# Optimization experiments

Measured on AMD Instinct MI355X. Metric: run time of the kernel, lower is better.

## Reference

```python
import jax, jax.numpy as jnp
import numpy as np

T, B = 10, 512
N_ALL, N_AGENTS = 23, 22
N_FEAT = 4
X_DIM = 4
Z_EACH = 4
Z_DIM = N_ALL * Z_EACH  # 92
RNN_H = 64
NH = 8
E = N_ALL * (N_ALL - 1)  # 506

# edge list equivalent of the dense one-hot rel_rec / rel_send matrices
_off = np.ones((N_ALL, N_ALL)) - np.eye(N_ALL)
_recv_np, _send_np = np.where(_off)
RECV = jnp.asarray(_recv_np)  # rel_rec one-hot rows -> receiver node ids
SEND = jnp.asarray(_send_np)  # rel_send one-hot rows -> sender node ids
_et = np.zeros((E, 2), np.float32)
_et[np.arange(0, E, N_ALL - 1)[1:-1], 0] = 1.0
_et[-(N_ALL - 1):, 1] = 1.0
EDGE_TYPE = jnp.asarray(_et)
_nt = np.zeros((N_ALL, 2), np.float32)
_nt[:-1, 0] = 1.0
_nt[-1, 1] = 1.0
NODE_TYPE = jnp.asarray(_nt)


def _bn(x, g, b):
    # BatchNorm1d in training mode over flattened (B*M, C), biased variance
    B_, M, C = x.shape
    xf = x.reshape(B_ * M, C)
    mu = xf.mean(0)
    var = jnp.var(xf, axis=0)
    return ((xf - mu) * jax.lax.rsqrt(var + 1e-5) * g + b).reshape(B_, M, C)


def _mlp(x, W1, b1, W2, b2, g, bt):
    h = jax.nn.elu(jnp.einsum('bmi,hi->bmh', x, W1) + b1)
    h = jax.nn.elu(jnp.einsum('bmi,hi->bmh', h, W2) + b2)
    return _bn(h, g, bt)


def _kld(me, se, mp_, sp):
    return 0.5 * jnp.sum(2.0 * jnp.log(sp / se) + (se ** 2 + (me - mp_) ** 2) / sp ** 2 - 1.0)


def _gru_cell(Wih, Whh, bih, bhh, x, h):
    gi = x @ Wih.T + bih
    gh = h @ Whh.T + bhh
    ir, iz, inn = jnp.split(gi, 3, -1)
    hr, hz, hn = jnp.split(gh, 3, -1)
    r = jax.nn.sigmoid(ir + hr)
    z = jax.nn.sigmoid(iz + hz)
    n = jnp.tanh(inn + r * hn)
    return (1.0 - z) * n + z * h


_gru = jax.vmap(_gru_cell)  # over agents


def _forward(states, eps, mlp1_W1, mlp1_b1, mlp1_W2, mlp1_b2, mlp1_g, mlp1_beta,
             mlp2_W1, mlp2_b1, mlp2_W2, mlp2_b2, mlp2_g, mlp2_beta,
             mlp3_W1, mlp3_b1, mlp3_W2, mlp3_b2, mlp3_g, mlp3_beta,
             enc_mean_W, enc_mean_b, enc_std_W, enc_std_b,
             prior_mean_W, prior_mean_b, prior_std_W, prior_std_b,
             dec_mean_W, dec_mean_b, dec_std_W, dec_std_b,
             gru_Wih, gru_Whh, gru_bih, gru_bhh):
    Bsz = states.shape[2]
    y = states[:T, 0].reshape(T, Bsz, N_ALL, N_FEAT)        # y_t
    x1 = states[1:T + 1, 0].reshape(T, Bsz, N_ALL, N_FEAT)  # x_{t+1}
    P1 = (mlp1_W1, mlp1_b1, mlp1_W2, mlp1_b2, mlp1_g, mlp1_beta)
    P2 = (mlp2_W1, mlp2_b1, mlp2_W2, mlp2_b2, mlp2_g, mlp2_beta)
    P3 = (mlp3_W1, mlp3_b1, mlp3_W2, mlp3_b2, mlp3_g, mlp3_beta)

    def gnn(x, p):
        x = _mlp(x, *(a[p] for a in P1))
        # node2edge: gather senders/receivers instead of one-hot matmul
        e = jnp.concatenate([x[:, SEND], x[:, RECV],
                             jnp.broadcast_to(EDGE_TYPE, (Bsz, E, 2))], -1)
        e = _mlp(e, *(a[p] for a in P2))
        # edge2node: scatter-add into receiver nodes (rel_rec.T @ e)
        inc = jnp.zeros((Bsz, N_ALL, NH), x.dtype).at[:, RECV].add(e)
        inc = jnp.concatenate([inc, jnp.broadcast_to(NODE_TYPE, (Bsz, N_ALL, 2))], -1) / N_ALL
        return _mlp(inc, *(a[p] for a in P3))

    def step(carry, xs):
        h, Lkl = carry
        y_t, x_t, eps_t = xs
        micro = jnp.transpose(h, (1, 0, 2)).reshape(Bsz, -1)  # (B, nA*H)
        pri = jnp.concatenate([gnn(y_t, 0).reshape(Bsz, -1), micro], 1)
        enc = jnp.concatenate([gnn(x_t, 1).reshape(Bsz, -1), micro], 1)
        pm = pri @ prior_mean_W.T + prior_mean_b
        ps = jax.nn.softplus(pri @ prior_std_W.T + prior_std_b)
        em = enc @ enc_mean_W.T + enc_mean_b
        es = jax.nn.softplus(enc @ enc_std_W.T + enc_std_b)
        z = em + es * eps_t  # reparameterized sample_gauss
        Lkl = Lkl + _kld(em, es, pm, ps)
        z_ = z.reshape(Bsz, N_ALL, Z_EACH)
        dg = gnn(z_, 2).reshape(Bsz, -1)
        dm = dg @ dec_mean_W.T + dec_mean_b
        ds = jax.nn.softplus(dg @ dec_std_W.T + dec_std_b)
        # per-agent GRU update: input = [x_t agent feats, z slice]
        gin = jnp.transpose(
            jnp.concatenate([x_t[:, :N_AGENTS, :X_DIM], z_[:, :N_AGENTS]], -1), (1, 0, 2))
        h = _gru(gru_Wih, gru_Whh, gru_bih, gru_bhh, gin, h)
        return (h, Lkl), (dm, ds)

    h0 = jnp.zeros((N_AGENTS, Bsz, RNN_H), states.dtype)
    (_, Lkl), (dms, dss) = jax.lax.scan(step, (h0, jnp.zeros((), states.dtype)), (y, x1, eps))
    return dms, dss, Lkl


def setup_inputs() -> dict:
    key = jax.random.key(0)
    ks = iter(jax.random.split(key, 64))

    def rn(shape, s=0.1):
        return jax.random.normal(next(ks), shape, jnp.float32) * s

    d = {}
    d['states'] = rn((T + 1, 1, B, N_ALL * N_FEAT), 1.0)
    d['eps'] = rn((T, B, Z_DIM), 1.0)
    for i, nin in ((1, N_FEAT), (2, 2 * NH + 2), (3, NH + 2)):
        d['mlp%d_W1' % i] = rn((3, NH, nin), 0.3)
        d['mlp%d_b1' % i] = jnp.full((3, NH), 0.1, jnp.float32)
        d['mlp%d_W2' % i] = rn((3, NH, NH), 0.3)
        d['mlp%d_b2' % i] = jnp.full((3, NH), 0.1, jnp.float32)
        d['mlp%d_g' % i] = jnp.ones((3, NH), jnp.float32)
        d['mlp%d_beta' % i] = jnp.zeros((3, NH), jnp.float32)
    IN_H = NH * N_ALL + RNN_H * N_AGENTS  # 1592
    for nm in ('enc_mean', 'enc_std', 'prior_mean', 'prior_std'):
        d[nm + '_W'] = rn((Z_DIM, IN_H), 0.02)
        d[nm + '_b'] = jnp.zeros((Z_DIM,), jnp.float32)
    OUT_DEC = NH * N_ALL  # 184
    for nm in ('dec_mean', 'dec_std'):
        d[nm + '_W'] = rn((X_DIM * N_AGENTS, OUT_DEC), 0.05)
        d[nm + '_b'] = jnp.zeros((X_DIM * N_AGENTS,), jnp.float32)
    d['gru_Wih'] = rn((N_AGENTS, 3 * RNN_H, X_DIM + Z_EACH), 0.2)
    d['gru_Whh'] = rn((N_AGENTS, 3 * RNN_H, RNN_H), 0.1)
    d['gru_bih'] = jnp.zeros((N_AGENTS, 3 * RNN_H), jnp.float32)
    d['gru_bhh'] = jnp.zeros((N_AGENTS, 3 * RNN_H), jnp.float32)
    return d


def reference(states, eps, mlp1_W1, mlp1_b1, mlp1_W2, mlp1_b2, mlp1_g, mlp1_beta,
              mlp2_W1, mlp2_b1, mlp2_W2, mlp2_b2, mlp2_g, mlp2_beta,
              mlp3_W1, mlp3_b1, mlp3_W2, mlp3_b2, mlp3_g, mlp3_beta,
              enc_mean_W, enc_mean_b, enc_std_W, enc_std_b,
              prior_mean_W, prior_mean_b, prior_std_W, prior_std_b,
              dec_mean_W, dec_mean_b, dec_std_W, dec_std_b,
              gru_Wih, gru_Whh, gru_bih, gru_bhh):
    return _forward(states, eps, mlp1_W1, mlp1_b1, mlp1_W2, mlp1_b2, mlp1_g, mlp1_beta,
                    mlp2_W1, mlp2_b1, mlp2_W2, mlp2_b2, mlp2_g, mlp2_beta,
                    mlp3_W1, mlp3_b1, mlp3_W2, mlp3_b2, mlp3_g, mlp3_beta,
                    enc_mean_W, enc_mean_b, enc_std_W, enc_std_b,
                    prior_mean_W, prior_mean_b, prior_std_W, prior_std_b,
                    dec_mean_W, dec_mean_b, dec_std_W, dec_std_b,
                    gru_Wih, gru_Whh, gru_bih, gru_bhh)
```

## Files before the change

kernel.cpp:

```cpp
#include <hip/hip_runtime.h>
#include <hip/hip_bf16.h>
#include <math.h>


typedef __attribute__((ext_vector_type(8))) short s16x8;
typedef __attribute__((ext_vector_type(4))) float f32x4;

__device__ __forceinline__ unsigned short f2bf(float x){
  __hip_bfloat16 b = __float2bfloat16(x);
  return *reinterpret_cast<unsigned short*>(&b);
}
__device__ __forceinline__ float elu_(float x){ return x>0.f ? x : __expf(x)-1.f; }
__device__ __forceinline__ float sp_(float x){ return fmaxf(x,0.f)+log1pf(__expf(-fabsf(x))); }
__device__ __forceinline__ float sig_(float x){ return 1.f/(1.f+__expf(-x)); }
__device__ __forceinline__ float wsum_(float v){
  #pragma unroll
  for (int o=32;o;o>>=1) v += __shfl_down(v,o,64);
  return v;
}

__device__ __forceinline__ void reduce_bn_(const float* __restrict__ part, int n,
    float invN, const float* __restrict__ gam, const float* __restrict__ bet,
    float* sc, float* sh, float* tmp)
{
// ... 17 lines not shown
    float s2 = rs*gam[tid];
    sc[tid] = s2; sh[tid] = bet[tid] - m*s2;
  }
  __syncthreads();
}

__device__ __forceinline__ void block_stats_(const float h[8], float* __restrict__ part,
                                             float red[][16])
{
  int wid = threadIdx.x >> 6, lane = threadIdx.x & 63;
  #pragma unroll
  for (int j=0;j<8;j++){
    float a = wsum_(h[j]);
    float b = wsum_(h[j]*h[j]);
    if (lane==0){ red[wid][j]=a; red[wid][8+j]=b; }
  }
  __syncthreads();
  if (threadIdx.x < 16)
    part[threadIdx.x] = red[0][threadIdx.x]+red[1][threadIdx.x]
                       +red[2][threadIdx.x]+red[3][threadIdx.x];
}


__device__ __forceinline__ void dev_heads_mfma(
    int idx, int t,
    const unsigned short* __restrict__ g3b,
    const unsigned short* __restrict__ hb,
    const unsigned short* __restrict__ Wbt,
    const unsigned short* __restrict__ Wbs,
    const float* __restrict__ cst,
    float* __restrict__ raw)
{
  int head = idx & 3, mb = idx >> 2;
  int tid = threadIdx.x;
  int wv = tid >> 6, lane = tid & 63;
  int m0 = mb*64 + wv*16;
  int rloc = lane & 15, kg = lane >> 4;
  int row = m0 + rloc;
  int selg = (head < 2) ? t : 10 + t;
  const unsigned short* Ag = g3b + (size_t)selg*98304 + (size_t)row*192 + kg*8;
  const unsigned short* Wt = Wbt + (size_t)((t*4+head)*96)*192 + kg*8;
  const unsigned short* Wsb = Wbs + (size_t)head*135168;
  f32x4 cd[6];
  #pragma unroll
  for (int n=0;n<6;n++) cd[n] = (f32x4){0.f,0.f,0.f,0.f};
  #pragma unroll
  for (int ks=0; ks<6; ks++){
    s16x8 af = *(const s16x8*)(Ag + ks*32);
    #pragma unroll
    for (int n=0;n<6;n++){
      int col = n*16 + rloc;
      s16x8 bf = *(const s16x8*)(Wt + (size_t)col*192 + ks*32);
      cd[n] = __builtin_amdgcn_mfma_f32_16x16x32_bf16(af, bf, cd[n], 0,0,0);
    }
  }
  const unsigned short* Ah = hb + (size_t)row*64;
  #pragma unroll 4
  for (int ks=0; ks<44; ks++){
    int f2 = ks*32 + kg*8;
    s16x8 af = *(const s16x8*)(Ah + (size_t)(f2>>6)*32768 + (f2&63));
    #pragma unroll
    for (int n=0;n<6;n++){
      int col = n*16 + rloc;
      s16x8 bf = *(const s16x8*)(Wsb + (size_t)col*1408 + f2);
      cd[n] = __builtin_amdgcn_mfma_f32_16x16x32_bf16(af, bf, cd[n], 0,0,0);
    }
  }
  float* dst = raw + (size_t)head*47104;
  const float* cb = cst + (size_t)(t*4+head)*96;
  #pragma unroll
  for (int n=0;n<6;n++){
    int col = n*16 + rloc;
    if (col < 92){
      float cc = cb[col];
      #pragma unroll
      for (int r=0;r<4;r++){
        int rr = m0 + (kg<<2) + r;
        dst[(size_t)rr*92 + col] = cd[n][r] + cc;
      }
    }
  }
}

__device__ __forceinline__ void dev_edges_z(
    float* smem, int b,
    const float* __restrict__ raw_prev, const float* __restrict__ eps_t,
    const float* __restrict__ bpm, const float* __restrict__ bps,
    const float* __restrict__ bem, const float* __restrict__ bes,
    const float* __restrict__ zp1,
    const float* __restrict__ nW1, const float* __restrict__ nb1,
    const float* __restrict__ nW2, const float* __restrict__ nb2,
    const float* __restrict__ g1, const float* __restrict__ bt1,
    const float* __restrict__ eW1, const float* __restrict__ eb1,
    const float* __restrict__ eW2, const float* __restrict__ eb2,
    float* __restrict__ zna, float* __restrict__ zp2, float* __restrict__ lklp_t)
{
  int tid = threadIdx.x;
  float* tmp   = smem;
  float* sc1   = smem+256;
  float* sh1   = smem+264;
  float* xnode = smem+272;
  float* accs  = smem+480;
  float* redsq = smem+688;
  float* zrow  = smem+720;
  float* redk  = smem+812;
  float* le    = smem+816;
  {
    int c = tid & 15, i0 = tid >> 4;
    float s = 0.f;
    for (int i=i0;i<368;i+=16) s += zp1[i*16+c];
    tmp[i0*16+c] = s;
    __syncthreads();
    if (tid<16){
      float v=0.f;
      #pragma unroll
      for (int i=0;i<16;i++) v += tmp[i*16+tid];
      tmp[tid]=v;
    }
    __syncthreads();
    if (tid<8){
      float m = tmp[tid]*(1.f/11776.f);
      float var = tmp[8+tid]*(1.f/11776.f) - m*m;
      float rs = rsqrtf(var+1e-5f);
      float s2 = rs*g1[tid];
      sc1[tid]=s2; sh1[tid]=bt1[tid]-m*s2;
    }
  }
  float kld = 0.f;
  if (tid < 92){
    int j = tid;
    const float* q = raw_prev + (size_t)b*92 + j;
    float pm = bpm[j] + q[0];
    float ps = sp_(bps[j] + q[47104]);
    float em = bem[j] + q[94208];
    float es = sp_(bes[j] + q[141312]);
    float z = em + es*eps_t[(size_t)b*92 + j];
    zrow[j] = z;
    float d = em - pm;
    kld = 0.5f*(2.f*logf(ps/es) + (es*es + d*d)/(ps*ps) - 1.f);
  }
  float kv = wsum_(kld);
  if ((tid&63)==0) redk[tid>>6] = kv;
  __syncthreads();
  if (tid==0) lklp_t[b] = redk[0]+redk[1]+redk[2]+redk[3];
  if (tid < 23){
    float z0=zrow[tid*4], z1=zrow[tid*4+1], z2=zrow[tid*4+2], z3=zrow[tid*4+3];
    float h1[8];
    #pragma unroll
    for (int j=0;j<8;j++)
      h1[j] = elu_(nb1[j] + nW1[j*4]*z0 + nW1[j*4+1]*z1 + nW1[j*4+2]*z2 + nW1[j*4+3]*z3);
    #pragma unroll
    for (int j=0;j<8;j++){
      float a = nb2[j];
      #pragma unroll
      for (int k=0;k<8;k++) a += nW2[j*8+k]*h1[k];
      xnode[tid*9+j] = elu_(a)*sc1[j] + sh1[j];
    }
  }
  __syncthreads();
  float sq[8]={0,0,0,0,0,0,0,0};
  for (int e=tid; e<506; e+=256){
    int r=e/22, jj=e-r*22;
    int s=jj+(jj>=r?1:0);
    float et0=(jj==0 && r>=1 && r<=21)?1.f:0.f;
    float et1=(r==22)?1.f:0.f;
    float h1[8];
    #pragma unroll
    for (int j=0;j<8;j++){
      const float* w=eW1+j*18;
      float a=eb1[j]+w[16]*et0+w[17]*et1;
      #pragma unroll
      for (int k=0;k<8;k++) a+=w[k]*xnode[s*9+k];
      #pragma unroll
      for (int k=0;k<8;k++) a+=w[8+k]*xnode[r*9+k];
      h1[j]=elu_(a);
    }
    #pragma unroll
    for (int j=0;j<8;j++){
      float a=eb2[j];
      #pragma unroll
      for (int k=0;k<8;k++) a+=eW2[j*8+k]*h1[k];
      float h2=elu_(a);
      le[e*9+j]=h2;
      sq[j]+=h2*h2;
    }
  }
  int wid=tid>>6, lane=tid&63;
  #pragma unroll
  for (int j=0;j<8;j++){
    float v=wsum_(sq[j]);
    if (lane==0) redsq[wid*8+j]=v;
  }
  __syncthreads();
  if (tid<184){
    int r=tid>>3, c=tid&7;
    const float* lp = le + r*198 + c;
    float s=0.f;
    #pragma unroll
    for (int jj=0;jj<22;jj++) s+=lp[jj*9];
    accs[r*9+c]=s;
    zna[(size_t)b*184+tid]=s;
  }
  __syncthreads();
  if (tid<16){
    int c=tid&7;
    float s=0.f;
    if (tid<8){
      #pragma unroll
      for (int r=0;r<23;r++) s+=accs[r*9+c];
    } else {
      #pragma unroll
      for (int w=0;w<4;w++) s+=redsq[w*8+c];
    }
    zp2[(size_t)b*16+tid]=s;
  }
}

__device__ __forceinline__ void dev_node3(
    float* smem, int bi, int g, int p,
    const float* __restrict__ nodeacc, const float* __restrict__ p2,
    const float* __restrict__ g2b, const float* __restrict__ bt2b,
    const float* __restrict__ W3b, const float* __restrict__ b3b,
    const float* __restrict__ W4b, const float* __restrict__ b4b,
    float* __restrict__ outf, unsigned short* __restrict__ outb,
    float* __restrict__ p3)
{
  float* tmp = smem; float* sc2 = smem+256; float* sh2 = smem+264;
  float (*red)[16] = (float(*)[16])(smem+272);
  reduce_bn_(p2 + (size_t)g*8192, 512, 1.f/259072.f, g2b+p*8, bt2b+p*8, sc2, sh2, tmp);
  int row = bi*256 + threadIdx.x;
  int b = row/23, r = row - b*23;
  const float inv23 = 1.f/23.f;
  const float* na = nodeacc + ((size_t)g*512 + b)*184 + r*8;
  float xk[8];
  #pragma unroll
  for (int k=0;k<8;k++) xk[k] = (na[k]*sc2[k] + 22.f*sh2[k]) * inv23;
  float nt0 = (r<22)?inv23:0.f, nt1 = (r==22)?inv23:0.f;
  const float* W3 = W3b + p*80; const float* b3 = b3b + p*8;
  const float* W4 = W4b + p*64; const float* b4 = b4b + p*8;
  float h1b[8], o[8];
  #pragma unroll
  for (int j=0;j<8;j++){
    const float* w = W3 + j*10;
    float a = b3[j] + w[8]*nt0 + w[9]*nt1;
    #pragma unroll
    for (int k=0;k<8;k++) a += w[k]*xk[k];
    h1b[j] = elu_(a);
  }
  #pragma unroll
  for (int j=0;j<8;j++){
    float a = b4[j];
    #pragma unroll
    for (int k=0;k<8;k++) a += W4[j*8+k]*h1b[k];
    o[j] = elu_(a);
    if (outf) outf[(size_t)row*8 + j] = o[j];
    else outb[(size_t)g*98304 + (size_t)b*192 + r*8 + j] = f2bf(o[j]);
  }
  block_stats_(o, p3 + ((size_t)g*46 + bi)*16, red);
}

__device__ __forceinline__ void dev_dec(
    float* smem, int bi,
    const float* __restrict__ zg3, const float* __restrict__ p3,
    const float* __restrict__ gam, const float* __restrict__ bet,
    const float* __restrict__ Wm, const float* __restrict__ Bm,
    const float* __restrict__ Wsd, const float* __restrict__ Bsd,
    float* __restrict__ odm, float* __restrict__ ods)
{
  int tid = threadIdx.x;
  float* dtmp = smem; float* dsc = smem + 256; float* dsh = smem + 264;
  reduce_bn_(p3, 46, 1.f/11776.f, gam, bet, dsc, dsh, dtmp);
  float4 s0 = {dsc[0],dsc[1],dsc[2],dsc[3]};
  float4 s1 = {dsc[4],dsc[5],dsc[6],dsc[7]};
  float4 t0 = {dsh[0],dsh[1],dsh[2],dsh[3]};
  float4 t1 = {dsh[4],dsh[5],dsh[6],dsh[7]};
  int idx = bi*256 + tid;
  int hd = idx / 45056; int rem = idx - hd*45056;
  int b = rem / 88, j = rem - b*88;
  const float* W = hd ? Wsd : Wm;
  const float4* a4 = (const float4*)(zg3 + (size_t)b*184);
  const float4* w4 = (const float4*)(W + (size_t)j*184);
  float accv = hd ? Bsd[j] : Bm[j];
  #pragma unroll 2
  for (int i4=0;i4<46;i4++){
    float4 x = a4[i4]; float4 w = w4[i4];
    float4 sc = (i4&1)? s1 : s0; float4 sh = (i4&1)? t1 : t0;
    accv += w.x*(x.x*sc.x+sh.x) + w.y*(x.y*sc.y+sh.y)
          + w.z*(x.z*sc.z+sh.z) + w.w*(x.w*sc.w+sh.w);
  }
  if (hd) ods[(size_t)b*88+j] = sp_(accv);
  else    odm[(size_t)b*88+j] = accv;
}

__device__ __forceinline__ void dev_gru_z(
    float* smem, int idx,
    float* __restrict__ h, unsigned short* __restrict__ hbf,
    const float* __restrict__ x_t,
    const float* __restrict__ raw_cur, const float* __restrict__ eps_t,
    const float* __restrict__ bem, const float* __restrict__ bes,
    const float* __restrict__ nW1, const float* __restrict__ nb1,
    const float* __restrict__ nW2, const float* __restrict__ nb2,
    float* __restrict__ zp1,
    const float* __restrict__ Wih, const float* __restrict__ Whh,
    const float* __restrict__ bih, const float* __restrict__ bhh)
{
  int tid = threadIdx.x;
  float* WhT  = smem;
  float* hs   = smem + 12352;
  float* gins = smem + 14656;
  int a = idx >> 4, yb = idx & 15;
  int b0 = yb*32;
  int c = tid & 63, sq = tid >> 6;
  const float* Wg = Whh + (size_t)a*12288;
  for (int e = tid; e < 12288; e += 256) WhT[(e&63)*193 + (e>>6)] = Wg[e];
  const float* hp_g = h + (size_t)a*32768 + (size_t)b0*64;
  for (int e = tid; e < 2048; e += 256) hs[(e&63)*36 + (e>>6)] = hp_g[e];
  { int s = tid >> 3, k = tid & 7;
    float v;
    if (k < 4) v = x_t[(size_t)(b0+s)*92 + a*4 + k];
    else {
      int j = a*4 + (k-4);
      float em = bem[j] + raw_cur[94208 + (size_t)(b0+s)*92 + j];
      float es = sp_(bes[j] + raw_cur[141312 + (size_t)(b0+s)*92 + j]);
      v = em + es*eps_t[(size_t)(b0+s)*92 + j];
    }
    gins[k*36 + s] = v; }
  float wi0[8], wi1[8], wi2[8];
  const float* Wig = Wih + (size_t)a*1536;
  #pragma unroll
  for (int k=0;k<8;k++){
    wi0[k] = Wig[c*8+k]; wi1[k] = Wig[(64+c)*8+k]; wi2[k] = Wig[(128+c)*8+k];
  }
  float bi0 = bih[a*192+c], bi1 = bih[a*192+64+c], bi2 = bih[a*192+128+c];
  float bh0 = bhh[a*192+c], bh1 = bhh[a*192+64+c], bh2 = bhh[a*192+128+c];
  __syncthreads();
  {
    float h2s[8];
    if (tid < 32){
      float z0=gins[4*36+tid], z1=gins[5*36+tid], z2=gins[6*36+tid], z3=gins[7*36+tid];
      float h1s[8];
      #pragma unroll
      for (int j=0;j<8;j++)
        h1s[j] = elu_(nb1[j] + nW1[j*4]*z0 + nW1[j*4+1]*z1 + nW1[j*4+2]*z2 + nW1[j*4+3]*z3);
      #pragma unroll
      for (int j=0;j<8;j++){
        float av = nb2[j];
        #pragma unroll
        for (int k=0;k<8;k++) av += nW2[j*8+k]*h1s[k];
        h2s[j] = elu_(av);
      }
    } else {
      #pragma unroll
      for (int j=0;j<8;j++) h2s[j] = 0.f;
    }
    float* dst = zp1 + (size_t)(a*16+yb)*16;
    #pragma unroll
    for (int j=0;j<8;j++){
      float s1 = wsum_(h2s[j]);
      float s2 = wsum_(h2s[j]*h2s[j]);
      if (tid==0){ dst[j]=s1; dst[8+j]=s2; }
    }
  }
  #pragma unroll
  for (int ps=0; ps<2; ps++){
    int s0 = ps*16 + sq*4;
    float q0[4], q1[4], q2[4];
    #pragma unroll
    for (int i=0;i<4;i++){ q0[i]=bh0; q1[i]=bh1; q2[i]=bh2; }
    for (int k=0;k<64;k++){
      float w0 = WhT[k*193 + c];
      float w1 = WhT[k*193 + 64 + c];
      float w2 = WhT[k*193 + 128 + c];
      float4 hv = *(const float4*)&hs[k*36 + s0];
      float hvv[4] = {hv.x,hv.y,hv.z,hv.w};
      #pragma unroll
      for (int i=0;i<4;i++){ q0[i]+=w0*hvv[i]; q1[i]+=w1*hvv[i]; q2[i]+=w2*hvv[i]; }
    }
    float g0[4], g1[4], g2[4];
    #pragma unroll
    for (int i=0;i<4;i++){ g0[i]=bi0; g1[i]=bi1; g2[i]=bi2; }
    #pragma unroll
    for (int k=0;k<8;k++){
      float4 gv = *(const float4*)&gins[k*36 + s0];
      float gvv[4] = {gv.x,gv.y,gv.z,gv.w};
      #pragma unroll
      for (int i=0;i<4;i++){ g0[i]+=wi0[k]*gvv[i]; g1[i]+=wi1[k]*gvv[i]; g2[i]+=wi2[k]*gvv[i]; }
    }
    float4 hp = *(const float4*)&hs[c*36 + s0];
    float hpv[4] = {hp.x,hp.y,hp.z,hp.w};
    #pragma unroll
    for (int i=0;i<4;i++){
      float rg = sig_(g0[i]+q0[i]);
      float zg = sig_(g1[i]+q1[i]);
      float ng = tanhf(g2[i] + rg*q2[i]);
      float hn = (1.f-zg)*ng + zg*hpv[i];
      size_t off = (size_t)a*32768 + (size_t)(b0+s0+i)*64 + c;
      h[off] = hn;
      hbf[off] = f2bf(hn);
    }
  }
}

__device__ __forceinline__ void dev_z22(
    int yb,
    const float* __restrict__ raw_cur, const float* __restrict__ eps_t,
    const float* __restrict__ bem, const float* __restrict__ bes,
    const float* __restrict__ nW1, const float* __restrict__ nb1,
    const float* __restrict__ nW2, const float* __restrict__ nb2,
    float* __restrict__ zp1)
{
  int tid = threadIdx.x;
  int b0 = yb*32;
  float h2s[8];
  if (tid < 32){
    float zv[4];
    #pragma unroll
    for (int q=0;q<4;q++){
      int j = 88+q;
      float em = bem[j] + raw_cur[94208 + (size_t)(b0+tid)*92 + j];
      float es = sp_(bes[j] + raw_cur[141312 + (size_t)(b0+tid)*92 + j]);
      zv[q] = em + es*eps_t[(size_t)(b0+tid)*92 + j];
    }
    float h1s[8];
    #pragma unroll
    for (int j=0;j<8;j++)
      h1s[j] = elu_(nb1[j] + nW1[j*4]*zv[0] + nW1[j*4+1]*zv[1] + nW1[j*4+2]*zv[2] + nW1[j*4+3]*zv[3]);
    #pragma unroll
    for (int j=0;j<8;j++){
      float av = nb2[j];
      #pragma unroll
      for (int k=0;k<8;k++) av += nW2[j*8+k]*h1s[k];
      h2s[j] = elu_(av);
    }
  } else {
    #pragma unroll
    for (int j=0;j<8;j++) h2s[j] = 0.f;
  }
  float* dst = zp1 + (size_t)(352+yb)*16;
  #pragma unroll
  for (int j=0;j<8;j++){
    float s1 = wsum_(h2s[j]);
    float s2 = wsum_(h2s[j]*h2s[j]);
    if (tid==0){ dst[j]=s1; dst[8+j]=s2; }
  }
}


__global__ __launch_bounds__(256) void k_stats1(
    const float* __restrict__ states,
    const float* __restrict__ W1b, const float* __restrict__ b1b,
    const float* __restrict__ W2b, const float* __restrict__ b2b,
    float* __restrict__ part)
{
  int g = blockIdx.y; int p = g/10; int t = g - p*10;
  const float* W1 = W1b + p*32; const float* b1 = b1b + p*8;
  const float* W2 = W2b + p*64; const float* b2 = b2b + p*8;
  int row = blockIdx.x*256 + threadIdx.x;
  float4 x4 = *(const float4*)(states + (size_t)(t+p)*47104 + 4*(size_t)row);
  float h1[8], h2[8];
  #pragma unroll
  for (int j=0;j<8;j++)
    h1[j] = elu_(b1[j] + W1[j*4+0]*x4.x + W1[j*4+1]*x4.y + W1[j*4+2]*x4.z + W1[j*4+3]*x4.w);
  #pragma unroll
  for (int j=0;j<8;j++){
    float a = b2[j];
    #pragma unroll
    for (int k=0;k<8;k++) a += W2[j*8+k]*h1[k];
    h2[j] = elu_(a);
  }
  __shared__ float red[4][16];
  block_stats_(h2, part + ((size_t)g*46 + blockIdx.x)*16, red);
}

__global__ __launch_bounds__(512) void k_pre_edges(
    const float* __restrict__ src, const float* __restrict__ p1,
    const float* __restrict__ nW1b, const float* __restrict__ nb1b,
    const float* __restrict__ nW2b, const float* __restrict__ nb2b,
    const float* __restrict__ g1b, const float* __restrict__ bt1b,
    const float* __restrict__ eW1b, const float* __restrict__ eb1b,
    const float* __restrict__ eW2b, const float* __restrict__ eb2b,
    float* __restrict__ nodeacc, float* __restrict__ p2)
{
  int g = blockIdx.y; int p = g/10; int t = g - p*10; int b = blockIdx.x;
  int tid = threadIdx.x;
  __shared__ float tmp[512];
  __shared__ float sc1[8], sh1[8];
  __shared__ float xnode[207];
  __shared__ float le[4554];
  __shared__ float accs[207];
  __shared__ float redsq[8][8];
  {
    const float* pp = p1 + (size_t)g*736;
    int c = tid & 15, i0 = tid >> 4;
    float s = 0.f;
    for (int i = i0; i < 46; i += 32) s += pp[i*16 + c];
    tmp[i0*16 + c] = s;
    __syncthreads();
    if (tid < 16){
      float v = 0.f;
      #pragma unroll
      for (int i=0;i<32;i++) v += tmp[i*16 + tid];
      tmp[tid] = v;
    }
    __syncthreads();
    if (tid < 8){
      float m = tmp[tid]*(1.f/11776.f);
      float var = tmp[8+tid]*(1.f/11776.f) - m*m;
      float rs = rsqrtf(var + 1e-5f);
      float s2 = rs*g1b[p*8+tid];
      sc1[tid] = s2; sh1[tid] = bt1b[p*8+tid] - m*s2;
    }
    __syncthreads();
  }
  if (tid < 23){
    const float* x = src + (size_t)(t+p)*47104 + (size_t)b*92 + tid*4;
    const float* W1 = nW1b + p*32; const float* b1 = nb1b + p*8;
    const float* W2 = nW2b + p*64; const float* b2 = nb2b + p*8;
    float x0=x[0], x1=x[1], x2=x[2], x3=x[3];
    float h1[8];
    #pragma unroll
    for (int j=0;j<8;j++)
      h1[j] = elu_(b1[j] + W1[j*4]*x0 + W1[j*4+1]*x1 + W1[j*4+2]*x2 + W1[j*4+3]*x3);
    #pragma unroll
    for (int j=0;j<8;j++){
      float a = b2[j];
      #pragma unroll
// ... 75 lines not shown
            nullptr, g3b, p3);
}

__global__ __launch_bounds__(256) void k_bnred(
    const float* __restrict__ part, int n, float invN,
    const float* __restrict__ gamb, const float* __restrict__ betb,
    float* __restrict__ scsh)
{
  int g = blockIdx.x; int p = g/10;
  int tid = threadIdx.x;
  __shared__ float tmp[256];
  const float* pp = part + (size_t)g*n*16;
  int c = tid & 15, i0 = tid >> 4;
  float s = 0.f;
  for (int i = i0; i < n; i += 16) s += pp[i*16 + c];
  tmp[i0*16 + c] = s;
  __syncthreads();
  if (tid < 16){
    float v = 0.f;
    #pragma unroll
    for (int i=0;i<16;i++) v += tmp[i*16 + tid];
    tmp[tid] = v;
  }
  __syncthreads();
  if (tid < 8){
    float m = tmp[tid]*invN;
    float var = tmp[8+tid]*invN - m*m;
    float rs = rsqrtf(var + 1e-5f);
    float sc = rs*gamb[p*8+tid];
    scsh[g*16 + tid] = sc;
    scsh[g*16 + 8 + tid] = betb[p*8+tid] - m*sc;
  }
}

__global__ __launch_bounds__(256) void k_wbs(
    const float* __restrict__ Wpm, const float* __restrict__ Wps,
    const float* __restrict__ Wem, const float* __restrict__ Wes,
    unsigned short* __restrict__ Wbs)
{
  int e = blockIdx.x*256 + threadIdx.x;
  int head = e / 135168; int rem = e - head*135168;
  int col = rem / 1408; int f2 = rem - col*1408;
  const float* W = (head==0)?Wpm:(head==1)?Wps:(head==2)?Wem:Wes;
  float v = (col<92) ? W[(size_t)col*1592 + 184 + f2] : 0.f;
  Wbs[e] = f2bf(v);
}

__global__ __launch_bounds__(256) void k_wbt(
    const float* __restrict__ Wpm, const float* __restrict__ Wps,
    const float* __restrict__ Wem, const float* __restrict__ Wes,
    const float* __restrict__ scsh3,
    unsigned short* __restrict__ Wbt)
{
  int e = blockIdx.x*256 + threadIdx.x;
  int t = e / 73728; int rem = e - t*73728;
  int head = rem / 18432; int rem2 = rem - head*18432;
  int col = rem2 / 192; int f = rem2 - col*192;
  const float* W = (head==0)?Wpm:(head==1)?Wps:(head==2)?Wem:Wes;
  int sel = (head<2) ? t : 10+t;
  float v = (col<92 && f<184) ? W[(size_t)col*1592 + f]*scsh3[sel*16 + (f&7)] : 0.f;
  Wbt[e] = f2bf(v);
}

__global__ __launch_bounds__(256) void k_cst(
    const float* __restrict__ Wpm, const float* __restrict__ Wps,
    const float* __restrict__ Wem, const float* __restrict__ Wes,
    const float* __restrict__ scsh3, float* __restrict__ cst)
{
  int e = blockIdx.x*256 + threadIdx.x;
  if (e >= 3840) return;
  int t = e / 384; int rem = e - t*384;
  int head = rem / 96; int col = rem - head*96;
  float s = 0.f;
  if (col < 92){
    const float* W = (head==0)?Wpm:(head==1)?Wps:(head==2)?Wem:Wes;
    int sel = (head<2) ? t : 10+t;
    const float* sh = scsh3 + sel*16 + 8;
    for (int f=0; f<184; f++) s += W[(size_t)col*1592+f]*sh[f&7];
  }
  cst[e] = s;
}


__global__ __launch_bounds__(256) void k_KA(
    int nh, int ne, int t,
    const unsigned short* __restrict__ g3b, const unsigned short* __restrict__ hbf,
    const unsigned short* __restrict__ Wbt, const unsigned short* __restrict__ Wbs,
    const float* __restrict__ cst, float* __restrict__ raw_cur,
    const float* __restrict__ raw_prev, const float* __restrict__ eps_prev,
    const float* __restrict__ bpm, const float* __restrict__ bps,
    const float* __restrict__ bem, const float* __restrict__ bes,
    const float* __restrict__ zp1,
    const float* __restrict__ nW1, const float* __restrict__ nb1,
    const float* __restrict__ nW2, const float* __restrict__ nb2,
    const float* __restrict__ g1, const float* __restrict__ bt1,
    const float* __restrict__ eW1, const float* __restrict__ eb1,
    const float* __restrict__ eW2, const float* __restrict__ eb2,
    float* __restrict__ zna, float* __restrict__ zp2, float* __restrict__ lklp_t,
    const float* __restrict__ zg3, const float* __restrict__ zp3,
    const float* __restrict__ gam3, const float* __restrict__ bet3,
    const float* __restrict__ Wm, const float* __restrict__ Bm,
    const float* __restrict__ Wsd, const float* __restrict__ Bsd,
    float* __restrict__ odm, float* __restrict__ ods)
{
  __shared__ float smem[5370];
  int it = blockIdx.x;
  if (it < nh)
    dev_heads_mfma(it, t, g3b, hbf, Wbt, Wbs, cst, raw_cur);
  else if (it < nh+ne)
    dev_edges_z(smem, it-nh, raw_prev, eps_prev, bpm,bps,bem,bes, zp1,
                nW1,nb1,nW2,nb2, g1,bt1, eW1,eb1,eW2,eb2, zna, zp2, lklp_t);
  else
    dev_dec(smem, it-nh-ne, zg3, zp3, gam3, bet3, Wm,Bm,Wsd,Bsd, odm, ods);
}

__global__ __launch_bounds__(256) void k_KB(
    int ng,
    float* __restrict__ h, unsigned short* __restrict__ hbf,
    const float* __restrict__ x_t,
    const float* __restrict__ raw_cur, const float* __restrict__ eps_t,
    const float* __restrict__ bem, const float* __restrict__ bes,
    const float* __restrict__ nW1, const float* __restrict__ nb1,
    const float* __restrict__ nW2, const float* __restrict__ nb2,
    float* __restrict__ zp1,
    const float* __restrict__ Wih, const float* __restrict__ Whh,
    const float* __restrict__ bih, const float* __restrict__ bhh,
    const float* __restrict__ zna, const float* __restrict__ zp2,
    const float* __restrict__ g2, const float* __restrict__ bt2,
    const float* __restrict__ W3, const float* __restrict__ b3,
    const float* __restrict__ W4, const float* __restrict__ b4,
    float* __restrict__ zg3, float* __restrict__ zp3)
{
  __shared__ float smem[14944];
  int it = blockIdx.x;
  if (it < ng){
    if (it < ng-16)
      dev_gru_z(smem, it, h, hbf, x_t, raw_cur, eps_t, bem, bes,
                nW1,nb1,nW2,nb2, zp1, Wih, Whh, bih, bhh);
    else
      dev_z22(it-(ng-16), raw_cur, eps_t, bem, bes, nW1,nb1,nW2,nb2, zp1);
  } else
    dev_node3(smem, it-ng, 0, 0, zna, zp2, g2, bt2, W3,b3,W4,b4,
              zg3, nullptr, zp3);
}

__global__ __launch_bounds__(256) void k_final(const float* __restrict__ lklp,
                                               float* __restrict__ out){
  __shared__ float red[4];
  float s = 0.f;
  for (int i = threadIdx.x; i < 5120; i += 256) s += lklp[i];
  s = wsum_(s);
  if ((threadIdx.x&63)==0) red[threadIdx.x>>6]=s;
  __syncthreads();
  if (threadIdx.x==0) out[0] = red[0]+red[1]+red[2]+red[3];
}

extern "C" void kernel_launch(void* const* d_in, const int* in_sizes, int n_in,
                              void* d_out, int out_size, void* d_ws, size_t ws_size,
                              hipStream_t stream)
{
  (void)in_sizes; (void)n_in; (void)out_size; (void)ws_size;
  const float* states=(const float*)d_in[0];
  const float* eps   =(const float*)d_in[1];
  const float *m1W1=(const float*)d_in[2],  *m1b1=(const float*)d_in[3],
              *m1W2=(const float*)d_in[4],  *m1b2=(const float*)d_in[5],
              *m1g =(const float*)d_in[6],  *m1bt=(const float*)d_in[7];
  const float *m2W1=(const float*)d_in[8],  *m2b1=(const float*)d_in[9],
              *m2W2=(const float*)d_in[10], *m2b2=(const float*)d_in[11],
              *m2g =(const float*)d_in[12], *m2bt=(const float*)d_in[13];
  const float *m3W1=(const float*)d_in[14], *m3b1=(const float*)d_in[15],
              *m3W2=(const float*)d_in[16], *m3b2=(const float*)d_in[17],
              *m3g =(const float*)d_in[18], *m3bt=(const float*)d_in[19];
  const float *emW=(const float*)d_in[20], *emB=(const float*)d_in[21];
  const float *esW=(const float*)d_in[22], *esB=(const float*)d_in[23];
  const float *pmW=(const float*)d_in[24], *pmB=(const float*)d_in[25];
  const float *psW=(const float*)d_in[26], *psB=(const float*)d_in[27];
  const float *dmW=(const float*)d_in[28], *dmB=(const float*)d_in[29];
  const float *dsW=(const float*)d_in[30], *dsB=(const float*)d_in[31];
  const float *gWih=(const float*)d_in[32], *gWhh=(const float*)d_in[33];
  const float *gbih=(const float*)d_in[34], *gbhh=(const float*)d_in[35];
  float* out = (float*)d_out;
  float* ws  = (float*)d_ws;

  unsigned short* g3b = (unsigned short*)(ws);
  unsigned short* Wbt = (unsigned short*)(ws + 983040);
  unsigned short* Wbs = (unsigned short*)(ws + 1351680);
  unsigned short* hbf = (unsigned short*)(ws + 1622016);
  float* h     = ws + 1982464;
  float* cst   = ws + 2703360;
  float* scsh3 = ws + 2707200;
  float* lklp  = ws + 2707520;
  float* zp1   = ws + 2712640;
  float* zna   = ws + 2718528;
  float* zp2   = ws + 2812736;
  float* zg3   = ws + 2820928;
  float* zp3   = ws + 2915136;
  float* raw0  = ws + 2915872;
  float* raw1  = ws + 3104288;
  float* scr   = ws + 3292704;
  float* p1p = scr;
  float* naP = scr + 14720;
  float* p2p = scr + 1898880;
  float* p3p = scr + 2062720;

  hipMemsetAsync(h, 0, 720896*sizeof(float), stream);
  hipMemsetAsync(hbf, 0, 720896*sizeof(unsigned short), stream);
  hipMemsetAsync(g3b, 0, 1966080*sizeof(unsigned short), stream);

  k_stats1<<<dim3(46,20),256,0,stream>>>(states, m1W1, m1b1, m1W2, m1b2, p1p);
  k_pre_edges<<<dim3(512,20),512,0,stream>>>(states, p1p,
      m1W1, m1b1, m1W2, m1b2, m1g, m1bt,
      m2W1, m2b1, m2W2, m2b2, naP, p2p);
  k_pre_node3<<<dim3(46,20),256,0,stream>>>(naP, p2p, m2g, m2bt,
      m3W1, m3b1, m3W2, m3b2, g3b, p3p);
  k_bnred<<<20,256,0,stream>>>(p3p, 46, 1.f/11776.f, m3g, m3bt, scsh3);
  k_wbs<<<2112,256,0,stream>>>(pmW, psW, emW, esW, Wbs);
  k_wbt<<<2880,256,0,stream>>>(pmW, psW, emW, esW, scsh3, Wbt);
  k_cst<<<15,256,0,stream>>>(pmW, psW, emW, esW, scsh3, cst);

  for (int t=0;t<=11;t++){
    int nh = (t<10)?32:0;
    int ne = (t>=1 && t<=10)?512:0;
    int nd = (t>=2)?352:0;
    int tt  = (t<10)? t : 0;
    int tm1 = (t>=1)? t-1 : 0;
    int tm2 = (t>=2)? t-2 : 0;
    float* rcur  = (t&1)? raw1 : raw0;
    float* rprev = (t&1)? raw0 : raw1;
    if (nh+ne+nd > 0)
      k_KA<<<nh+ne+nd,256,0,stream>>>(nh, ne, tt,
          g3b, hbf, Wbt, Wbs, cst, rcur,
          rprev, eps + (size_t)tm1*47104,
          pmB, psB, emB, esB, zp1,
          m1W1+64, m1b1+16, m1W2+128, m1b2+16, m1g+16, m1bt+16,
          m2W1+288, m2b1+16, m2W2+128, m2b2+16,
          zna, zp2, lklp + (size_t)tm1*512,
          zg3, zp3, m3g+16, m3bt+16, dmW, dmB, dsW, dsB,
          out + (size_t)tm2*45056, out + 450560 + (size_t)tm2*45056);
    int ng = (t<10)?368:0;
    int nn = (t>=1 && t<=10)?46:0;
    if (ng+nn > 0)
      k_KB<<<ng+nn,256,0,stream>>>(ng,
          h, hbf, states + (size_t)((t<10)? t+1 : 1)*47104,
          rcur, eps + (size_t)tt*47104,
          emB, esB, m1W1+64, m1b1+16, m1W2+128, m1b2+16, zp1,
          gWih, gWhh, gbih, gbhh,
          zna, zp2, m2g+16, m2bt+16,
          m3W1+160, m3b1+16, m3W2+128, m3b2+16, zg3, zp3);
  }
  k_final<<<1,256,0,stream>>>(lklp, out + 901120);
}
```

Baseline: 975.5 us.

## Compute z and KLD once per step in a fused kernel, restructure recurrent schedule

Reparameterised z, KLD and the first node-MLP statistics are now computed once per step in a dedicated fused stage and stored to a z buffer. Before, the edge, GRU and z22 paths each recomputed them. The per-step schedule changes from two kernels to three (heads+edges, fused z/node3, GRU+decoder), and the double-buffered raw output becomes a single buffer. This removes redundant softplus/exp work and lets the decoder run one step earlier, at the cost of an extra launch per timestep.

```diff
diff --git a/kernel.cpp b/kernel.cpp
--- a/kernel.cpp
+++ b/kernel.cpp
@@ -123,18 +123,14 @@
   }
 }
 
-__device__ __forceinline__ void dev_edges_z(
-    float* smem, int b,
-    const float* __restrict__ raw_prev, const float* __restrict__ eps_t,
-    const float* __restrict__ bpm, const float* __restrict__ bps,
-    const float* __restrict__ bem, const float* __restrict__ bes,
-    const float* __restrict__ zp1,
+__device__ __forceinline__ void dev_edges(
+    float* smem, int b, const float* __restrict__ zb, const float* __restrict__ p1,
     const float* __restrict__ nW1, const float* __restrict__ nb1,
     const float* __restrict__ nW2, const float* __restrict__ nb2,
     const float* __restrict__ g1, const float* __restrict__ bt1,
     const float* __restrict__ eW1, const float* __restrict__ eb1,
     const float* __restrict__ eW2, const float* __restrict__ eb2,
-    float* __restrict__ zna, float* __restrict__ zp2, float* __restrict__ lklp_t)
+    float* __restrict__ zna, float* __restrict__ zp2)
 {
   int tid = threadIdx.x;
   float* tmp   = smem;
@@ -143,13 +139,11 @@
   float* xnode = smem+272;
   float* accs  = smem+480;
   float* redsq = smem+688;
-  float* zrow  = smem+720;
-  float* redk  = smem+812;
-  float* le    = smem+816;
+  float* le    = smem+720;
   {
     int c = tid & 15, i0 = tid >> 4;
     float s = 0.f;
-    for (int i=i0;i<368;i+=16) s += zp1[i*16+c];
+    for (int i=i0;i<46;i+=16) s += p1[i*16+c];
     tmp[i0*16+c] = s;
     __syncthreads();
     if (tid<16){
@@ -166,36 +160,21 @@
       float s2 = rs*g1[tid];
       sc1[tid]=s2; sh1[tid]=bt1[tid]-m*s2;
     }
-  }
-  float kld = 0.f;
-  if (tid < 92){
-    int j = tid;
-    const float* q = raw_prev + (size_t)b*92 + j;
-    float pm = bpm[j] + q[0];
-    float ps = sp_(bps[j] + q[47104]);
-    float em = bem[j] + q[94208];
-    float es = sp_(bes[j] + q[141312]);
-    float z = em + es*eps_t[(size_t)b*92 + j];
-    zrow[j] = z;
-    float d = em - pm;
-    kld = 0.5f*(2.f*logf(ps/es) + (es*es + d*d)/(ps*ps) - 1.f);
-  }
-  float kv = wsum_(kld);
-  if ((tid&63)==0) redk[tid>>6] = kv;
-  __syncthreads();
-  if (tid==0) lklp_t[b] = redk[0]+redk[1]+redk[2]+redk[3];
-  if (tid < 23){
-    float z0=zrow[tid*4], z1=zrow[tid*4+1], z2=zrow[tid*4+2], z3=zrow[tid*4+3];
+    __syncthreads();
+  }
+  if (tid<23){
+    const float* x = zb + (size_t)b*92 + tid*4;
+    float x0=x[0],x1=x[1],x2=x[2],x3=x[3];
     float h1[8];
     #pragma unroll
     for (int j=0;j<8;j++)
-      h1[j] = elu_(nb1[j] + nW1[j*4]*z0 + nW1[j*4+1]*z1 + nW1[j*4+2]*z2 + nW1[j*4+3]*z3);
+      h1[j]=elu_(nb1[j]+nW1[j*4]*x0+nW1[j*4+1]*x1+nW1[j*4+2]*x2+nW1[j*4+3]*x3);
     #pragma unroll
     for (int j=0;j<8;j++){
-      float a = nb2[j];
-      #pragma unroll
-      for (int k=0;k<8;k++) a += nW2[j*8+k]*h1[k];
-      xnode[tid*9+j] = elu_(a)*sc1[j] + sh1[j];
+      float a=nb2[j];
+      #pragma unroll
+      for (int k=0;k<8;k++) a+=nW2[j*8+k]*h1[k];
+      xnode[tid*9+j]=elu_(a)*sc1[j]+sh1[j];
     }
   }
   __syncthreads();
@@ -205,15 +184,18 @@
     int s=jj+(jj>=r?1:0);
     float et0=(jj==0 && r>=1 && r<=21)?1.f:0.f;
     float et1=(r==22)?1.f:0.f;
+    float xs[8], xr[8];
+    #pragma unroll
+    for (int k=0;k<8;k++){ xs[k]=xnode[s*9+k]; xr[k]=xnode[r*9+k]; }
     float h1[8];
     #pragma unroll
     for (int j=0;j<8;j++){
       const float* w=eW1+j*18;
       float a=eb1[j]+w[16]*et0+w[17]*et1;
       #pragma unroll
-      for (int k=0;k<8;k++) a+=w[k]*xnode[s*9+k];
-      #pragma unroll
-      for (int k=0;k<8;k++) a+=w[8+k]*xnode[r*9+k];
+      for (int k=0;k<8;k++) a+=w[k]*xs[k];
+      #pragma unroll
+      for (int k=0;k<8;k++) a+=w[8+k]*xr[k];
       h1[j]=elu_(a);
     }
     #pragma unroll
@@ -298,6 +280,65 @@
     else outb[(size_t)g*98304 + (size_t)b*192 + r*8 + j] = f2bf(o[j]);
   }
   block_stats_(o, p3 + ((size_t)g*46 + bi)*16, red);
+}
+
+__device__ __forceinline__ void dev_fused(
+    float* smem, int bi,
+    const float* __restrict__ raw,
+    const float* __restrict__ bpm, const float* __restrict__ bps,
+    const float* __restrict__ bem, const float* __restrict__ bes,
+    const float* __restrict__ eps_t, float* __restrict__ z,
+    float* __restrict__ lklp,
+    const float* __restrict__ W1, const float* __restrict__ b1,
+    const float* __restrict__ W2, const float* __restrict__ b2,
+    float* __restrict__ part)
+{
+  float* redk = smem;
+  float (*red)[16] = (float(*)[16])(smem+4);
+  int tid = threadIdx.x;
+  int row = bi*256 + tid;
+  int bb = row/23, n = row - bb*23;
+  (void)bb;
+  float4 a  = *(const float4*)(raw + 4*(size_t)row);
+  float4 bq = *(const float4*)(raw + 47104 + 4*(size_t)row);
+  float4 c  = *(const float4*)(raw + 94208 + 4*(size_t)row);
+  float4 d  = *(const float4*)(raw + 141312 + 4*(size_t)row);
+  float pm[4]={a.x,a.y,a.z,a.w}, ps[4]={bq.x,bq.y,bq.z,bq.w};
+  float em[4]={c.x,c.y,c.z,c.w}, es[4]={d.x,d.y,d.z,d.w};
+  int j0 = 4*n;
+  float4 e4 = *(const float4*)(eps_t + 4*(size_t)row);
+  float ev[4] = {e4.x, e4.y, e4.z, e4.w};
+  float zv[4]; float kl = 0.f;
+  #pragma unroll
+  for (int q=0;q<4;q++){
+    float PM = pm[q] + bpm[j0+q];
+    float PS = sp_(ps[q] + bps[j0+q]);
+    float EM = em[q] + bem[j0+q];
+    float ES = sp_(es[q] + bes[j0+q]);
+    zv[q] = EM + ES*ev[q];
+    float dd = EM - PM;
+    kl += 0.5f*(2.f*logf(PS/ES) + (ES*ES + dd*dd)/(PS*PS) - 1.f);
+  }
+  float4 zq; zq.x=zv[0]; zq.y=zv[1]; zq.z=zv[2]; zq.w=zv[3];
+  *(float4*)(z + 4*(size_t)row) = zq;
+  float ks = wsum_(kl);
+  if ((tid&63)==0) redk[tid>>6] = ks;
+  __syncthreads();
+  if (tid==0) lklp[bi] = redk[0]+redk[1]+redk[2]+redk[3];
+  float h1[8], h2[8];
+  #pragma unroll
+  for (int j=0;j<8;j++){
+    float av = b1[j] + W1[j*4+0]*zv[0] + W1[j*4+1]*zv[1] + W1[j*4+2]*zv[2] + W1[j*4+3]*zv[3];
+    h1[j] = elu_(av);
+  }
+  #pragma unroll
+  for (int j=0;j<8;j++){
+    float av = b2[j];
+    #pragma unroll
+    for (int k=0;k<8;k++) av += W2[j*8+k]*h1[k];
+    h2[j] = elu_(av);
+  }
+  block_stats_(h2, part + (size_t)bi*16, red);
 }
 
 __device__ __forceinline__ void dev_dec(
@@ -333,17 +374,13 @@
   else    odm[(size_t)b*88+j] = accv;
 }
 
-__device__ __forceinline__ void dev_gru_z(
+__device__ __forceinline__ void dev_gru(
     float* smem, int idx,
     float* __restrict__ h, unsigned short* __restrict__ hbf,
     const float* __restrict__ x_t,
-    const float* __restrict__ raw_cur, const float* __restrict__ eps_t,
-    const float* __restrict__ bem, const float* __restrict__ bes,
-    const float* __restrict__ nW1, const float* __restrict__ nb1,
-    const float* __restrict__ nW2, const float* __restrict__ nb2,
-    float* __restrict__ zp1,
-    const float* __restrict__ Wih, const float* __restrict__ Whh,
-    const float* __restrict__ bih, const float* __restrict__ bhh)
+    const float* __restrict__ z, const float* __restrict__ Wih,
+    const float* __restrict__ Whh, const float* __restrict__ bih,
+    const float* __restrict__ bhh)
 {
   int tid = threadIdx.x;
   float* WhT  = smem;
@@ -357,14 +394,8 @@
   const float* hp_g = h + (size_t)a*32768 + (size_t)b0*64;
   for (int e = tid; e < 2048; e += 256) hs[(e&63)*36 + (e>>6)] = hp_g[e];
   { int s = tid >> 3, k = tid & 7;
-    float v;
-    if (k < 4) v = x_t[(size_t)(b0+s)*92 + a*4 + k];
-    else {
-      int j = a*4 + (k-4);
-      float em = bem[j] + raw_cur[94208 + (size_t)(b0+s)*92 + j];
-      float es = sp_(bes[j] + raw_cur[141312 + (size_t)(b0+s)*92 + j]);
-      v = em + es*eps_t[(size_t)(b0+s)*92 + j];
-    }
+    float v = (k<4) ? x_t[(size_t)(b0+s)*92 + a*4 + k]
+                    : z[(size_t)(b0+s)*92 + a*4 + (k-4)];
     gins[k*36 + s] = v; }
   float wi0[8], wi1[8], wi2[8];
   const float* Wig = Wih + (size_t)a*1536;
@@ -375,33 +406,6 @@
   float bi0 = bih[a*192+c], bi1 = bih[a*192+64+c], bi2 = bih[a*192+128+c];
   float bh0 = bhh[a*192+c], bh1 = bhh[a*192+64+c], bh2 = bhh[a*192+128+c];
   __syncthreads();
-  {
-    float h2s[8];
-    if (tid < 32){
-      float z0=gins[4*36+tid], z1=gins[5*36+tid], z2=gins[6*36+tid], z3=gins[7*36+tid];
-      float h1s[8];
-      #pragma unroll
-      for (int j=0;j<8;j++)
-        h1s[j] = elu_(nb1[j] + nW1[j*4]*z0 + nW1[j*4+1]*z1 + nW1[j*4+2]*z2 + nW1[j*4+3]*z3);
-      #pragma unroll
-      for (int j=0;j<8;j++){
-        float av = nb2[j];
-        #pragma unroll
-        for (int k=0;k<8;k++) av += nW2[j*8+k]*h1s[k];
-        h2s[j] = elu_(av);
-      }
-    } else {
-      #pragma unroll
-      for (int j=0;j<8;j++) h2s[j] = 0.f;
-    }
-    float* dst = zp1 + (size_t)(a*16+yb)*16;
-    #pragma unroll
-    for (int j=0;j<8;j++){
-      float s1 = wsum_(h2s[j]);
-      float s2 = wsum_(h2s[j]*h2s[j]);
-      if (tid==0){ dst[j]=s1; dst[8+j]=s2; }
-    }
-  }
   #pragma unroll
   for (int ps=0; ps<2; ps++){
     int s0 = ps*16 + sq*4;
@@ -439,50 +443,6 @@
       h[off] = hn;
       hbf[off] = f2bf(hn);
     }
-  }
-}
-
-__device__ __forceinline__ void dev_z22(
-    int yb,
-    const float* __restrict__ raw_cur, const float* __restrict__ eps_t,
-    const float* __restrict__ bem, const float* __restrict__ bes,
-    const float* __restrict__ nW1, const float* __restrict__ nb1,
-    const float* __restrict__ nW2, const float* __restrict__ nb2,
-    float* __restrict__ zp1)
-{
-  int tid = threadIdx.x;
-  int b0 = yb*32;
-  float h2s[8];
-  if (tid < 32){
-    float zv[4];
-    #pragma unroll
-    for (int q=0;q<4;q++){
-      int j = 88+q;
-      float em = bem[j] + raw_cur[94208 + (size_t)(b0+tid)*92 + j];
-      float es = sp_(bes[j] + raw_cur[141312 + (size_t)(b0+tid)*92 + j]);
-      zv[q] = em + es*eps_t[(size_t)(b0+tid)*92 + j];
-    }
-    float h1s[8];
-    #pragma unroll
-    for (int j=0;j<8;j++)
-      h1s[j] = elu_(nb1[j] + nW1[j*4]*zv[0] + nW1[j*4+1]*zv[1] + nW1[j*4+2]*zv[2] + nW1[j*4+3]*zv[3]);
-    #pragma unroll
-    for (int j=0;j<8;j++){
-      float av = nb2[j];
-      #pragma unroll
-      for (int k=0;k<8;k++) av += nW2[j*8+k]*h1s[k];
-      h2s[j] = elu_(av);
-    }
-  } else {
-    #pragma unroll
-    for (int j=0;j<8;j++) h2s[j] = 0.f;
-  }
-  float* dst = zp1 + (size_t)(352+yb)*16;
-  #pragma unroll
-  for (int j=0;j<8;j++){
-    float s1 = wsum_(h2s[j]);
-    float s2 = wsum_(h2s[j]*h2s[j]);
-    if (tid==0){ dst[j]=s1; dst[8+j]=s2; }
   }
 }
 
@@ -724,73 +684,76 @@
 }
 
 
-__global__ __launch_bounds__(256) void k_KA(
-    int nh, int ne, int t,
+__global__ __launch_bounds__(256) void k_K1(
+    int nh, int t,
     const unsigned short* __restrict__ g3b, const unsigned short* __restrict__ hbf,
     const unsigned short* __restrict__ Wbt, const unsigned short* __restrict__ Wbs,
-    const float* __restrict__ cst, float* __restrict__ raw_cur,
-    const float* __restrict__ raw_prev, const float* __restrict__ eps_prev,
-    const float* __restrict__ bpm, const float* __restrict__ bps,
-    const float* __restrict__ bem, const float* __restrict__ bes,
-    const float* __restrict__ zp1,
+    const float* __restrict__ cst, float* __restrict__ raw,
+    const float* __restrict__ zb, const float* __restrict__ zp1,
     const float* __restrict__ nW1, const float* __restrict__ nb1,
     const float* __restrict__ nW2, const float* __restrict__ nb2,
     const float* __restrict__ g1, const float* __restrict__ bt1,
     const float* __restrict__ eW1, const float* __restrict__ eb1,
     const float* __restrict__ eW2, const float* __restrict__ eb2,
-    float* __restrict__ zna, float* __restrict__ zp2, float* __restrict__ lklp_t,
-    const float* __restrict__ zg3, const float* __restrict__ zp3,
-    const float* __restrict__ gam3, const float* __restrict__ bet3,
-    const float* __restrict__ Wm, const float* __restrict__ Bm,
-    const float* __restrict__ Wsd, const float* __restrict__ Bsd,
-    float* __restrict__ odm, float* __restrict__ ods)
-{
-  __shared__ float smem[5370];
-  int it = blockIdx.x;
-  if (it < nh)
-    dev_heads_mfma(it, t, g3b, hbf, Wbt, Wbs, cst, raw_cur);
-  else if (it < nh+ne)
-    dev_edges_z(smem, it-nh, raw_prev, eps_prev, bpm,bps,bem,bes, zp1,
-                nW1,nb1,nW2,nb2, g1,bt1, eW1,eb1,eW2,eb2, zna, zp2, lklp_t);
+    float* __restrict__ zna, float* __restrict__ zp2)
+{
+  __shared__ float smem[5274];
+  if ((int)blockIdx.x < nh)
+    dev_heads_mfma(blockIdx.x, t, g3b, hbf, Wbt, Wbs, cst, raw);
   else
-    dev_dec(smem, it-nh-ne, zg3, zp3, gam3, bet3, Wm,Bm,Wsd,Bsd, odm, ods);
-}
-
-__global__ __launch_bounds__(256) void k_KB(
-    int ng,
-    float* __restrict__ h, unsigned short* __restrict__ hbf,
-    const float* __restrict__ x_t,
-    const float* __restrict__ raw_cur, const float* __restrict__ eps_t,
+    dev_edges(smem, blockIdx.x - nh, zb, zp1,
+              nW1,nb1,nW2,nb2, g1,bt1, eW1,eb1,eW2,eb2, zna, zp2);
+}
+
+__global__ __launch_bounds__(256) void k_K2(
+    int nf,
+    const float* __restrict__ raw,
+    const float* __restrict__ bpm, const float* __restrict__ bps,
     const float* __restrict__ bem, const float* __restrict__ bes,
-    const float* __restrict__ nW1, const float* __restrict__ nb1,
-    const float* __restrict__ nW2, const float* __restrict__ nb2,
-    float* __restrict__ zp1,
-    const float* __restrict__ Wih, const float* __restrict__ Whh,
-    const float* __restrict__ bih, const float* __restrict__ bhh,
+    const float* __restrict__ eps_t, float* __restrict__ z,
+    float* __restrict__ lklp,
+    const float* __restrict__ W1, const float* __restrict__ b1,
+    const float* __restrict__ W2, const float* __restrict__ b2,
+    float* __restrict__ part,
     const float* __restrict__ zna, const float* __restrict__ zp2,
     const float* __restrict__ g2, const float* __restrict__ bt2,
     const float* __restrict__ W3, const float* __restrict__ b3,
     const float* __restrict__ W4, const float* __restrict__ b4,
     float* __restrict__ zg3, float* __restrict__ zp3)
 {
+  __shared__ float smem[336];
+  if ((int)blockIdx.x < nf)
+    dev_fused(smem, blockIdx.x, raw, bpm,bps,bem,bes, eps_t, z, lklp, W1,b1,W2,b2, part);
+  else
+    dev_node3(smem, blockIdx.x - nf, 0, 0, zna, zp2, g2, bt2, W3,b3,W4,b4,
+              zg3, nullptr, zp3);
+}
+
+__global__ __launch_bounds__(256) void k_K3(
+    int ngru,
+    float* __restrict__ h, unsigned short* __restrict__ hbf,
+    const float* __restrict__ x_t,
+    const float* __restrict__ z, const float* __restrict__ Wih,
+    const float* __restrict__ Whh, const float* __restrict__ bih,
+    const float* __restrict__ bhh,
+    const float* __restrict__ zg3, const float* __restrict__ p3,
+    const float* __restrict__ gam, const float* __restrict__ bet,
+    const float* __restrict__ Wm, const float* __restrict__ Bm,
+    const float* __restrict__ Wsd, const float* __restrict__ Bsd,
+    float* __restrict__ odm, float* __restrict__ ods)
+{
   __shared__ float smem[14944];
-  int it = blockIdx.x;
-  if (it < ng){
-    if (it < ng-16)
-      dev_gru_z(smem, it, h, hbf, x_t, raw_cur, eps_t, bem, bes,
-                nW1,nb1,nW2,nb2, zp1, Wih, Whh, bih, bhh);
-    else
-      dev_z22(it-(ng-16), raw_cur, eps_t, bem, bes, nW1,nb1,nW2,nb2, zp1);
-  } else
-    dev_node3(smem, it-ng, 0, 0, zna, zp2, g2, bt2, W3,b3,W4,b4,
-              zg3, nullptr, zp3);
+  if ((int)blockIdx.x < ngru)
+    dev_gru(smem, blockIdx.x, h, hbf, x_t, z, Wih, Whh, bih, bhh);
+  else
+    dev_dec(smem, blockIdx.x - ngru, zg3, p3, gam, bet, Wm,Bm,Wsd,Bsd, odm, ods);
 }
 
 __global__ __launch_bounds__(256) void k_final(const float* __restrict__ lklp,
                                                float* __restrict__ out){
   __shared__ float red[4];
   float s = 0.f;
-  for (int i = threadIdx.x; i < 5120; i += 256) s += lklp[i];
+  for (int i = threadIdx.x; i < 460; i += 256) s += lklp[i];
   s = wsum_(s);
   if ((threadIdx.x&63)==0) red[threadIdx.x>>6]=s;
   __syncthreads();
@@ -831,15 +794,15 @@
   float* h     = ws + 1982464;
   float* cst   = ws + 2703360;
   float* scsh3 = ws + 2707200;
-  float* lklp  = ws + 2707520;
-  float* zp1   = ws + 2712640;
-  float* zna   = ws + 2718528;
-  float* zp2   = ws + 2812736;
-  float* zg3   = ws + 2820928;
-  float* zp3   = ws + 2915136;
-  float* raw0  = ws + 2915872;
-  float* raw1  = ws + 3104288;
-  float* scr   = ws + 3292704;
+  float* zb    = ws + 2707520;
+  float* lklp  = ws + 2754624;
+  float* zp1   = ws + 2755088;
+  float* zna   = ws + 2755824;
+  float* zp2   = ws + 2850032;
+  float* zg3   = ws + 2858224;
+  float* zp3   = ws + 2952432;
+  float* raw   = ws + 2953168;
+  float* scr   = ws + 3141584;
   float* p1p = scr;
   float* naP = scr + 14720;
   float* p2p = scr + 1898880;
@@ -860,35 +823,30 @@
   k_wbt<<<2880,256,0,stream>>>(pmW, psW, emW, esW, scsh3, Wbt);
   k_cst<<<15,256,0,stream>>>(pmW, psW, emW, esW, scsh3, cst);
 
-  for (int t=0;t<=11;t++){
-    int nh = (t<10)?32:0;
-    int ne = (t>=1 && t<=10)?512:0;
-    int nd = (t>=2)?352:0;
-    int tt  = (t<10)? t : 0;
-    int tm1 = (t>=1)? t-1 : 0;
-    int tm2 = (t>=2)? t-2 : 0;
-    float* rcur  = (t&1)? raw1 : raw0;
-    float* rprev = (t&1)? raw0 : raw1;
-    if (nh+ne+nd > 0)
-      k_KA<<<nh+ne+nd,256,0,stream>>>(nh, ne, tt,
-          g3b, hbf, Wbt, Wbs, cst, rcur,
-          rprev, eps + (size_t)tm1*47104,
-          pmB, psB, emB, esB, zp1,
+  for (int t=0;t<=10;t++){
+    int nh = (t<10)?32:0, ne = (t>0)?512:0;
+    int tt = (t<10)? t : 0;
+    if (nh+ne > 0)
+      k_K1<<<nh+ne,256,0,stream>>>(nh, tt,
+          g3b, hbf, Wbt, Wbs, cst, raw,
+          zb, zp1,
           m1W1+64, m1b1+16, m1W2+128, m1b2+16, m1g+16, m1bt+16,
-          m2W1+288, m2b1+16, m2W2+128, m2b2+16,
-          zna, zp2, lklp + (size_t)tm1*512,
-          zg3, zp3, m3g+16, m3bt+16, dmW, dmB, dsW, dsB,
-          out + (size_t)tm2*45056, out + 450560 + (size_t)tm2*45056);
-    int ng = (t<10)?368:0;
-    int nn = (t>=1 && t<=10)?46:0;
-    if (ng+nn > 0)
-      k_KB<<<ng+nn,256,0,stream>>>(ng,
-          h, hbf, states + (size_t)((t<10)? t+1 : 1)*47104,
-          rcur, eps + (size_t)tt*47104,
-          emB, esB, m1W1+64, m1b1+16, m1W2+128, m1b2+16, zp1,
-          gWih, gWhh, gbih, gbhh,
+          m2W1+288, m2b1+16, m2W2+128, m2b2+16, zna, zp2);
+    int nf = (t<10)?46:0, nn = (t>0)?46:0;
+    if (nf+nn > 0)
+      k_K2<<<nf+nn,256,0,stream>>>(nf,
+          raw, pmB, psB, emB, esB,
+          eps + (size_t)tt*47104, zb, lklp + tt*46,
+          m1W1+64, m1b1+16, m1W2+128, m1b2+16, zp1,
           zna, zp2, m2g+16, m2bt+16,
           m3W1+160, m3b1+16, m3W2+128, m3b2+16, zg3, zp3);
+    int ng = (t<10)?352:0, nd = (t>0)?352:0;
+    int tm1 = (t>0)? t-1 : 0;
+    if (ng+nd > 0)
+      k_K3<<<ng+nd,256,0,stream>>>(ng,
+          h, hbf, states + (size_t)(tt+1)*47104, zb, gWih, gWhh, gbih, gbhh,
+          zg3, zp3, m3g+16, m3bt+16, dmW, dmB, dsW, dsB,
+          out + (size_t)tm1*45056, out + 450560 + (size_t)tm1*45056);
   }
   k_final<<<1,256,0,stream>>>(lklp, out + 901120);
 }
```

New measurement: 1.011 ms. 1.04x slower.
